# Kernel tuning notes

Measured on AMD Instinct MI355X. Metric: run time of the kernel, lower is better.

Reference implementation:

```python
import jax, jax.numpy as jnp
import numpy as np

TOP_K = 3
EPS = 1e-12  # F.normalize eps


def _lstm(x, W_ih, W_hh, b_ih, b_hh):
    # x: [B, S, I]; PyTorch gate order i, f, g, o; returns h sequence [B, S, H]
    B = x.shape[0]
    H = W_hh.shape[1]
    xs = jnp.swapaxes(x, 0, 1)  # [S, B, I]
    x_proj = xs @ W_ih.T + b_ih + b_hh  # [S, B, 4H]

    def step(carry, xp):
        h, c = carry
        gates = xp + h @ W_hh.T
        i, f, g, o = jnp.split(gates, 4, axis=-1)
        i = jax.nn.sigmoid(i); f = jax.nn.sigmoid(f)
        g = jnp.tanh(g); o = jax.nn.sigmoid(o)
        c = f * c + i * g
        h = o * jnp.tanh(c)
        return (h, c), h

    init = (jnp.zeros((B, H), x.dtype), jnp.zeros((B, H), x.dtype))
    _, hs = jax.lax.scan(step, init, x_proj)
    return jnp.swapaxes(hs, 0, 1)  # [B, S, H]


def setup_inputs() -> dict:
    key = jax.random.key(0)
    ks = jax.random.split(key, 16)
    B, S, I, H, M, N, O = 4, 256, 512, 1024, 256, 65536, 512
    sc = 0.02
    return {
        "x": jax.random.normal(ks[0], (B, S, I), jnp.float32),
        "keys": jax.random.normal(ks[1], (N, M), jnp.float32),
        "values": jax.random.normal(ks[2], (N, M), jnp.float32),
        "importance": jnp.ones((N,), jnp.float32),
        "W_ih": jax.random.normal(ks[3], (4 * H, I), jnp.float32) * sc,
        "W_hh": jax.random.normal(ks[4], (4 * H, H), jnp.float32) * sc,
        "b_ih": jnp.zeros((4 * H,), jnp.float32),
        "b_hh": jnp.zeros((4 * H,), jnp.float32),
        "Wq": jax.random.normal(ks[5], (M, H), jnp.float32) * sc,
        "bq": jnp.zeros((M,), jnp.float32),
        "Wa": jax.random.normal(ks[6], (1, M), jnp.float32) * sc,
        "ba": jnp.zeros((1,), jnp.float32),
        "Wc": jax.random.normal(ks[7], (M, M), jnp.float32) * sc,
        "bc": jnp.zeros((M,), jnp.float32),
        "Wo": jax.random.normal(ks[8], (O, H + M), jnp.float32) * sc,
        "bo": jnp.zeros((O,), jnp.float32),
    }


def reference(x, keys, values, importance, W_ih, W_hh, b_ih, b_hh,
              Wq, bq, Wa, ba, Wc, bc, Wo, bo):
    # Controller LSTM over the whole sequence
    h = _lstm(x, W_ih, W_hh, b_ih, b_hh)  # [B, S, H]

    # Query projection and cosine similarity against the memory keys
    q = h @ Wq.T + bq  # [B, S, M]
    qn = q / jnp.maximum(jnp.linalg.norm(q, axis=-1, keepdims=True), EPS)
    kn = keys / jnp.maximum(jnp.linalg.norm(keys, axis=-1, keepdims=True), EPS)
    sim = jnp.einsum("bsm,nm->bsn", qn, kn) * importance  # [B, S, N]

    # Top-k retrieval and value gather
    _, top_idx = jax.lax.top_k(sim, TOP_K)  # [B, S, k]
    retrieved = values[top_idx]  # [B, S, k, M]

    # Learned attention over retrieved memories
    att_logits = (retrieved @ Wa.T + ba)[..., 0]  # [B, S, k]
    att = jax.nn.softmax(att_logits, axis=-1)
    mem = jnp.einsum("bsk,bskm->bsm", att, retrieved)
    mem = mem @ Wc.T + bc  # combine_layer

    out = jnp.concatenate([h, mem], axis=-1) @ Wo.T + bo  # [B, S, O]
    return out
```

## Files before the change

### kernel.cpp

```cpp
#include <hip/hip_runtime.h>
#include <hip/hip_bf16.h>
#include <cstdint>
#include <cstddef>

#define BB 4
#define SS 256
#define ID 512
#define HD 1024
#define MD 256
#define NKEY 65536
#define OD 512
#define ROWS 1024
#define NWG_LSTM 256
#define NTH_LSTM 256
#define KPB 2048
#define KSPLITS (NKEY / KPB)

typedef __attribute__((ext_vector_type(8))) short bf16x8;
typedef __attribute__((ext_vector_type(4))) float f32x4;
typedef __attribute__((ext_vector_type(8))) unsigned short u16x8;

__global__ __launch_bounds__(256) void sgemm_nt(
    const float* __restrict__ A, int lda,
    const float* __restrict__ Bm, int ldb,
    float* __restrict__ C, int ldc, int K,
    const float* __restrict__ bias, const float* __restrict__ bias2,
    int accum)
{
    __shared__ float As[64][17];
    __shared__ float Bs[64][17];
    const int t = threadIdx.x;
    const int tx = t & 15, ty = t >> 4;
    const int bm = blockIdx.y << 6, bn = blockIdx.x << 6;
    const int lrow = t >> 2, lk4 = (t & 3) << 2;
    float acc[4][4] = {};

    for (int kb = 0; kb < K; kb += 16) {
        const float4 av = *(const float4*)&A[(size_t)(bm + lrow) * lda + kb + lk4];
        const float4 bv = *(const float4*)&Bm[(size_t)(bn + lrow) * ldb + kb + lk4];
        __syncthreads();
        As[lrow][lk4 + 0] = av.x; As[lrow][lk4 + 1] = av.y;
        As[lrow][lk4 + 2] = av.z; As[lrow][lk4 + 3] = av.w;
        Bs[lrow][lk4 + 0] = bv.x; Bs[lrow][lk4 + 1] = bv.y;
        Bs[lrow][lk4 + 2] = bv.z; Bs[lrow][lk4 + 3] = bv.w;
        __syncthreads();
#pragma unroll
        for (int k = 0; k < 16; ++k) {
            const float a0 = As[4 * ty + 0][k], a1 = As[4 * ty + 1][k];
            const float a2 = As[4 * ty + 2][k], a3 = As[4 * ty + 3][k];
            const float b0 = Bs[4 * tx + 0][k], b1 = Bs[4 * tx + 1][k];
            const float b2 = Bs[4 * tx + 2][k], b3 = Bs[4 * tx + 3][k];
            acc[0][0] += a0 * b0; acc[0][1] += a0 * b1; acc[0][2] += a0 * b2; acc[0][3] += a0 * b3;
            acc[1][0] += a1 * b0; acc[1][1] += a1 * b1; acc[1][2] += a1 * b2; acc[1][3] += a1 * b3;
            acc[2][0] += a2 * b0; acc[2][1] += a2 * b1; acc[2][2] += a2 * b2; acc[2][3] += a2 * b3;
            acc[3][0] += a3 * b0; acc[3][1] += a3 * b1; acc[3][2] += a3 * b2; acc[3][3] += a3 * b3;
        }
    }

#pragma unroll
    for (int i = 0; i < 4; ++i) {
        const int row = bm + 4 * ty + i;
        const int col = bn + 4 * tx;
        float4* cp = (float4*)&C[(size_t)row * ldc + col];
        float4 r;
        if (accum) {
            const float4 old = *cp;
            r.x = old.x + acc[i][0]; r.y = old.y + acc[i][1];
            r.z = old.z + acc[i][2]; r.w = old.w + acc[i][3];
        } else {
            float bx = bias[col + 0], by = bias[col + 1], bz = bias[col + 2], bw = bias[col + 3];
            if (bias2) { bx += bias2[col + 0]; by += bias2[col + 1]; bz += bias2[col + 2]; bw += bias2[col + 3]; }
            r.x = acc[i][0] + bx; r.y = acc[i][1] + by;
            r.z = acc[i][2] + bz; r.w = acc[i][3] + bw;
        }
        *cp = r;
    }
}

__global__ __launch_bounds__(256) void sgemm_nt_w(
    const float* __restrict__ A, const float* __restrict__ Bm,
    float* __restrict__ C, const float* __restrict__ bias, const float* __restrict__ bias2)
{
    __shared__ float As[16][64];
    __shared__ float Bs[16][128];
    const int t = threadIdx.x;
    const int tx = t & 15, ty = t >> 4;
    const int bm = blockIdx.y << 6, bn = blockIdx.x << 7;
    const int arow = t & 63, akq = t >> 6;
    const int brow = t & 127, bkq = t >> 7;
    float acc[4][8] = {};

    for (int kb = 0; kb < 512; kb += 16) {
        const float4 av  = *(const float4*)&A[(size_t)(bm + arow) * 512 + kb + (akq << 2)];
        const float4 bv0 = *(const float4*)&Bm[(size_t)(bn + brow) * 512 + kb + (bkq << 3)];
        const float4 bv1 = *(const float4*)&Bm[(size_t)(bn + brow) * 512 + kb + (bkq << 3) + 4];
        __syncthreads();
        As[(akq << 2) + 0][arow] = av.x; As[(akq << 2) + 1][arow] = av.y;
        As[(akq << 2) + 2][arow] = av.z; As[(akq << 2) + 3][arow] = av.w;
        Bs[(bkq << 3) + 0][brow] = bv0.x; Bs[(bkq << 3) + 1][brow] = bv0.y;
        Bs[(bkq << 3) + 2][brow] = bv0.z; Bs[(bkq << 3) + 3][brow] = bv0.w;
        Bs[(bkq << 3) + 4][brow] = bv1.x; Bs[(bkq << 3) + 5][brow] = bv1.y;
        Bs[(bkq << 3) + 6][brow] = bv1.z; Bs[(bkq << 3) + 7][brow] = bv1.w;
        __syncthreads();
#pragma unroll
        for (int k = 0; k < 16; ++k) {
            const float4 a  = *(const float4*)&As[k][ty << 2];
            const float4 b0 = *(const float4*)&Bs[k][tx << 3];
            const float4 b1 = *(const float4*)&Bs[k][(tx << 3) + 4];
            acc[0][0] += a.x * b0.x; acc[0][1] += a.x * b0.y; acc[0][2] += a.x * b0.z; acc[0][3] += a.x * b0.w;
            acc[0][4] += a.x * b1.x; acc[0][5] += a.x * b1.y; acc[0][6] += a.x * b1.z; acc[0][7] += a.x * b1.w;
            acc[1][0] += a.y * b0.x; acc[1][1] += a.y * b0.y; acc[1][2] += a.y * b0.z; acc[1][3] += a.y * b0.w;
            acc[1][4] += a.y * b1.x; acc[1][5] += a.y * b1.y; acc[1][6] += a.y * b1.z; acc[1][7] += a.y * b1.w;
            acc[2][0] += a.z * b0.x; acc[2][1] += a.z * b0.y; acc[2][2] += a.z * b0.z; acc[2][3] += a.z * b0.w;
            acc[2][4] += a.z * b1.x; acc[2][5] += a.z * b1.y; acc[2][6] += a.z * b1.z; acc[2][7] += a.z * b1.w;
            acc[3][0] += a.w * b0.x; acc[3][1] += a.w * b0.y; acc[3][2] += a.w * b0.z; acc[3][3] += a.w * b0.w;
            acc[3][4] += a.w * b1.x; acc[3][5] += a.w * b1.y; acc[3][6] += a.w * b1.z; acc[3][7] += a.w * b1.w;
        }
    }

#pragma unroll
    for (int i = 0; i < 4; ++i) {
        const int row = bm + (ty << 2) + i;
        const int col = bn + (tx << 3);
        float4 r0, r1;
        r0.x = acc[i][0] + bias[col + 0] + bias2[col + 0];
        r0.y = acc[i][1] + bias[col + 1] + bias2[col + 1];
        r0.z = acc[i][2] + bias[col + 2] + bias2[col + 2];
        r0.w = acc[i][3] + bias[col + 3] + bias2[col + 3];
        r1.x = acc[i][4] + bias[col + 4] + bias2[col + 4];
        r1.y = acc[i][5] + bias[col + 5] + bias2[col + 5];
        r1.z = acc[i][6] + bias[col + 6] + bias2[col + 6];
        r1.w = acc[i][7] + bias[col + 7] + bias2[col + 7];
        *(float4*)&C[(size_t)row * 4096 + col] = r0;
        *(float4*)&C[(size_t)row * 4096 + col + 4] = r1;
    }
}

__device__ inline unsigned pack_bf16(float a, float b) {
    return (__float_as_uint(a) >> 16) | (__float_as_uint(b) & 0xFFFF0000u);
}

__global__ void rownorm(const float* __restrict__ X, float* __restrict__ Xn, int nrows)
{
    const int row = blockIdx.x * 4 + (threadIdx.x >> 6);
    const int lane = threadIdx.x & 63;
    if (row >= nrows) return;
    float4 v = *(const float4*)&X[(size_t)row * 256 + (lane << 2)];
    float ss = v.x * v.x + v.y * v.y + v.z * v.z + v.w * v.w;
#pragma unroll
    for (int o = 1; o < 64; o <<= 1) ss += __shfl_xor(ss, o);
    const float sc = 1.f / fmaxf(sqrtf(ss), 1e-12f);
    v.x *= sc; v.y *= sc; v.z *= sc; v.w *= sc;
    *(float4*)&Xn[(size_t)row * 256 + (lane << 2)] = v;
}

__device__ inline float sigm_f(float x) { return 1.f / (1.f + __expf(-x)); }
__device__ inline float tanh_f(float x) { return 1.f - 2.f / (__expf(2.f * x) + 1.f); }

#define SUBSTEP(B, U, UN, C4, XPC) do {                                           \
    asm volatile("s_waitcnt vmcnt(3)" ::: "memory");                              \
    __builtin_amdgcn_sched_barrier(0);                                            \
    const unsigned* pb_ = rec + (slot << 12) + (B << 10) + (t << 2);              \
    while ((((U.x ^ st) | (U.y ^ st) | (U.z ^ st) | (U.w ^ st)) & 0xFFu) != 0u) { \
        __builtin_amdgcn_s_sleep(1);                                              \
        asm volatile("global_load_dwordx4 %0, %1, off sc0 sc1\n\ts_waitcnt vmcnt(0)" \
                     : "=&v"(U) : "v"(pb_) : "memory");                           \
    }                                                                             \
    {                                                                             \
        float4 hw_;                                                               \
        hw_.x = __uint_as_float(U.x & 0xFFFFFF00u);                               \
        hw_.y = __uint_as_float(U.y & 0xFFFFFF00u);                               \
        hw_.z = __uint_as_float(U.z & 0xFFFFFF00u);                               \
        hw_.w = __uint_as_float(U.w & 0xFFFFFF00u);                               \
        *(float4*)&h_lds[B][t << 2] = hw_;                                        \
    }                                                                             \
    asm volatile("s_waitcnt lgkmcnt(0)" ::: "memory");                            \
    __builtin_amdgcn_sched_barrier(0);                                            \
    __builtin_amdgcn_s_barrier();                                                 \
    {                                                                             \
        const unsigned* pn_ = rec + (((B == 3) ? (slot ^ 1) : slot) << 12)        \
                              + (((B + 1) & 3) << 10) + (t << 2);                 \
        asm volatile("global_load_dwordx4 %0, %1, off sc0 sc1"                    \
                     : "=&v"(UN) : "v"(pn_) : "memory");                          \
    }                                                                             \
    const float* hb_ = &h_lds[B][0];                                              \
    float ax_ = 0.f, ay_ = 0.f, az_ = 0.f, aw_ = 0.f;                             \
    _Pragma("unroll")                                                             \
    for (int j = 0; j < 16; ++j) {                                                \
        const float4 hv_ = *(const float4*)&hb_[(ksub << 2) + (j << 6)];          \
        ax_ += w4[j].x * hv_.x; ay_ += w4[j].y * hv_.y;                           \
        az_ += w4[j].z * hv_.z; aw_ += w4[j].w * hv_.w;                           \
    }                                                                             \
    float sm_ = (ax_ + ay_) + (az_ + aw_);                                        \
    sm_ += __shfl_xor(sm_, 1); sm_ += __shfl_xor(sm_, 2);                         \
    sm_ += __shfl_xor(sm_, 4); sm_ += __shfl_xor(sm_, 8);                         \
    sm_ += XPC;                                                                   \
    const float vi_ = __shfl(sm_, ksub);                                          \
    const float vf_ = __shfl(sm_, ksub + 16);                                     \
    const float vg_ = __shfl(sm_, ksub + 32);                                     \
    const float vo_ = __shfl(sm_, ksub + 48);                                     \
    const float iv_ = sigm_f(vi_), fv_ = sigm_f(vf_);                             \
    const float gv_ = tanh_f(vg_), ov_ = sigm_f(vo_);                             \
    C4 = fv_ * C4 + iv_ * gv_;                                                    \
    const float hvv_ = ov_ * tanh_f(C4);                                          \
    if (lane == 0) {                                                              \
        unsigned* dst_ = rec + ((slot ^ 1) << 12) + (B << 10) + unit;             \
        const unsigned uv_ = (__float_as_uint(hvv_) & 0xFFFFFF00u) |              \
                             ((unsigned)(s + 1) & 0xFFu);                         \
        float* ha_ = &h_all[(size_t)((B << 8) + s) * 1024 + unit];                \
        asm volatile("global_store_dword %0, %1, off sc0 sc1"                     \
                     :: "v"(dst_), "v"(uv_) : "memory");                          \
        asm volatile("global_store_dword %0, %1, off"                             \
                     :: "v"(ha_), "v"(hvv_) : "memory");                          \
    }                                                                             \
    {                                                                             \
        const float* px_ = &xp[(size_t)((B << 8) + sn) * 4096 + wrow];            \
        asm volatile("global_load_dword %0, %1, off"                              \
                     : "=&v"(XPC) : "v"(px_) : "memory");                         \
    }                                                                             \
} while (0)

__global__ __launch_bounds__(256) void lstm_kernel(
    const float* __restrict__ xp, const float* __restrict__ W_hh,
    unsigned* __restrict__ rec, float* __restrict__ h_all,
    const float* __restrict__ keys, const float* __restrict__ imp,
    float* __restrict__ rnk, unsigned short* __restrict__ kb)
{
    __shared__ float h_lds[4][1024];
    const int t = threadIdx.x;

    if (blockIdx.x >= NWG_LSTM) {
        const int base_row = (blockIdx.x - NWG_LSTM) << 8;
        const int lane = t & 63;
        for (int it = 0; it < 64; ++it) {
            const int row = base_row + (it << 2) + (t >> 6);
            float4 v = *(const float4*)&keys[(size_t)row * 256 + (lane << 2)];
            float ss = v.x * v.x + v.y * v.y + v.z * v.z + v.w * v.w;
#pragma unroll
            for (int o = 1; o < 64; o <<= 1) ss += __shfl_xor(ss, o);
            const float sc = imp[row] / fmaxf(sqrtf(ss), 1e-12f);
            if (lane == 0) rnk[row] = sc;
            if (kb) {
                uint2 p;
                p.x = pack_bf16(v.x * sc, v.y * sc);
                p.y = pack_bf16(v.z * sc, v.w * sc);
                *(uint2*)&kb[(size_t)row * 256 + (lane << 2)] = p;
            }
        }
        return;
    }

    const int wave = t >> 6, lane = t & 63;
    const int gt = lane >> 4, ksub = lane & 15;
    const int unit = (blockIdx.x << 2) + wave;
    const int wrow = (gt << 10) + unit;

    float4 w4[16];
#pragma unroll
    for (int j = 0; j < 16; ++j)
        w4[j] = *(const float4*)&W_hh[(size_t)wrow * 1024 + (ksub << 2) + (j << 6)];

    float c40 = 0.f, c41 = 0.f, c42 = 0.f, c43 = 0.f;
    float xpc0 = xp[(size_t)(0 * 256 + 0) * 4096 + wrow];
    float xpc1 = xp[(size_t)(1 * 256 + 0) * 4096 + wrow];
    float xpc2 = xp[(size_t)(2 * 256 + 0) * 4096 + wrow];
    float xpc3 = xp[(size_t)(3 * 256 + 0) * 4096 + wrow];

    uint4 u0 = make_uint4(~0u, ~0u, ~0u, ~0u);
    uint4 u1 = u0, u2 = u0, u3 = u0;

    {
        const unsigned* p00 = rec + (t << 2);
        asm volatile("global_load_dwordx4 %0, %1, off sc0 sc1\n\ts_waitcnt vmcnt(0)"
                     : "=&v"(u0) : "v"(p00) : "memory");
        __builtin_amdgcn_sched_barrier(0);
    }

    for (int s = 0; s < 256; ++s) {
        const int slot = s & 1;
        const unsigned st = (unsigned)s & 0xFFu;
        const int sn = (s < 255) ? s + 1 : 255;
        SUBSTEP(0, u0, u1, c40, xpc0);
        SUBSTEP(1, u1, u2, c41, xpc1);
        SUBSTEP(2, u2, u3, c42, xpc2);
        SUBSTEP(3, u3, u0, c43, xpc3);
    }
}

#define SWAP1(A, B, IA, IB) { float _t = A; A = B; B = _t; int _u = IA; IA = IB; IB = _u; }
#define INS8G(P, V, ID) do {                                          \
    const float _v = (V); const int _id = (ID);                       \
    if (_v > P##v7) {                                                 \
        P##v7 = _v; P##i7 = _id;                                      \
        if (P##v7 > P##v6) SWAP1(P##v6, P##v7, P##i6, P##i7);         \
        if (P##v6 > P##v5) SWAP1(P##v5, P##v6, P##i5, P##i6);         \
        if (P##v5 > P##v4) SWAP1(P##v4, P##v5, P##i4, P##i5);         \
        if (P##v4 > P##v3) SWAP1(P##v3, P##v4, P##i3, P##i4);         \
        if (P##v3 > P##v2) SWAP1(P##v2, P##v3, P##i2, P##i3);         \
        if (P##v2 > P##v1) SWAP1(P##v1, P##v2, P##i1, P##i2);         \
        if (P##v1 > P##v0) SWAP1(P##v0, P##v1, P##i0, P##i1);         \
    }                                                                 \
} while (0)
#define DECL8(P) float P##v0=-3e38f,P##v1=-3e38f,P##v2=-3e38f,P##v3=-3e38f, \
                       P##v4=-3e38f,P##v5=-3e38f,P##v6=-3e38f,P##v7=-3e38f; \
                 int P##i0=0x7fffffff,P##i1=0x7fffffff,P##i2=0x7fffffff,P##i3=0x7fffffff, \
                     P##i4=0x7fffffff,P##i5=0x7fffffff,P##i6=0x7fffffff,P##i7=0x7fffffff;

__global__ __launch_bounds__(256) void sim_mfma_b(
    const float* __restrict__ qn, const unsigned short* __restrict__ kb,
    float* __restrict__ part_v8, int* __restrict__ part_i8)
{
    __shared__ unsigned short k_lds[64 * 264];
    __shared__ float cand_v[256 * 8];
    __shared__ int   cand_i[256 * 8];
    const int t = threadIdx.x;
    const int wave = t >> 6, lane = t & 63;
    const int ks = blockIdx.x, qs = blockIdx.y;
    const int key_base = ks * KPB;
    const int q0 = qs << 6;
    const int qrow = q0 + (wave << 4) + (lane & 15);
    const int kg = lane >> 4;

    bf16x8 bq[8];
#pragma unroll
    for (int kc = 0; kc < 8; ++kc) {
        const float* qp = &qn[(size_t)qrow * 256 + (kc << 5) + (kg << 3)];
        const float4 f0 = *(const float4*)qp;
        const float4 f1 = *(const float4*)(qp + 4);
        union { unsigned int u[4]; bf16x8 h; } cv;
        cv.u[0] = pack_bf16(f0.x, f0.y);
        cv.u[1] = pack_bf16(f0.z, f0.w);
        cv.u[2] = pack_bf16(f1.x, f1.y);
        cv.u[3] = pack_bf16(f1.z, f1.w);
        bq[kc] = cv.h;
    }

    DECL8(t)

    const int srow = t >> 2, scol0 = (t & 3) << 6;

    for (int stg = 0; stg < KPB / 64; ++stg) {
        __syncthreads();
        {
            const unsigned short* kp = &kb[(size_t)(key_base + (stg << 6) + srow) * 256 + scol0];
#pragma unroll
            for (int i = 0; i < 8; ++i)
                *(u16x8*)&k_lds[srow * 264 + scol0 + (i << 3)] = *(const u16x8*)(kp + (i << 3));
        }
        __syncthreads();

#pragma unroll
        for (int kt = 0; kt < 4; ++kt) {
            f32x4 a0 = {0.f, 0.f, 0.f, 0.f};
            f32x4 a1 = {0.f, 0.f, 0.f, 0.f};
#pragma unroll
            for (int kc = 0; kc < 4; ++kc) {
                const bf16x8 af = *(const bf16x8*)&k_lds[((kt << 4) + (lane & 15)) * 264 +
                                                         (kc << 5) + (kg << 3)];
                a0 = __builtin_amdgcn_mfma_f32_16x16x32_bf16(af, bq[kc], a0, 0, 0, 0);
            }
#pragma unroll
            for (int kc = 4; kc < 8; ++kc) {
                const bf16x8 af = *(const bf16x8*)&k_lds[((kt << 4) + (lane & 15)) * 264 +
                                                         (kc << 5) + (kg << 3)];
                a1 = __builtin_amdgcn_mfma_f32_16x16x32_bf16(af, bq[kc], a1, 0, 0, 0);
            }
            const int kidx = key_base + (stg << 6) + (kt << 4) + (kg << 2);
            INS8G(t, a0[0] + a1[0], kidx + 0);
            INS8G(t, a0[1] + a1[1], kidx + 1);
            INS8G(t, a0[2] + a1[2], kidx + 2);
            INS8G(t, a0[3] + a1[3], kidx + 3);
        }
    }

    __syncthreads();
    cand_v[t * 8 + 0] = tv0; cand_i[t * 8 + 0] = ti0;
    cand_v[t * 8 + 1] = tv1; cand_i[t * 8 + 1] = ti1;
    cand_v[t * 8 + 2] = tv2; cand_i[t * 8 + 2] = ti2;
    cand_v[t * 8 + 3] = tv3; cand_i[t * 8 + 3] = ti3;
    cand_v[t * 8 + 4] = tv4; cand_i[t * 8 + 4] = ti4;
    cand_v[t * 8 + 5] = tv5; cand_i[t * 8 + 5] = ti5;
    cand_v[t * 8 + 6] = tv6; cand_i[t * 8 + 6] = ti6;
    cand_v[t * 8 + 7] = tv7; cand_i[t * 8 + 7] = ti7;
    __syncthreads();
    if (t < 64) {
        DECL8(m)
        const int w = t >> 4, c = t & 15;
        for (int g = 0; g < 4; ++g) {
            const int src = ((w << 6) + c + (g << 4)) * 8;
            for (int r = 0; r < 8; ++r)
                INS8G(m, cand_v[src + r], cand_i[src + r]);
        }
        const size_t base = (size_t)(q0 + t) * (KSPLITS * 8) + ks * 8;
        part_v8[base + 0] = mv0; part_i8[base + 0] = mi0;
        part_v8[base + 1] = mv1; part_i8[base + 1] = mi1;
        part_v8[base + 2] = mv2; part_i8[base + 2] = mi2;
        part_v8[base + 3] = mv3; part_i8[base + 3] = mi3;
        part_v8[base + 4] = mv4; part_i8[base + 4] = mi4;
        part_v8[base + 5] = mv5; part_i8[base + 5] = mi5;
        part_v8[base + 6] = mv6; part_i8[base + 6] = mi6;
        part_v8[base + 7] = mv7; part_i8[base + 7] = mi7;
    }
}

__global__ __launch_bounds__(256) void sim_mfma_f(
    const float* __restrict__ qn, const float* __restrict__ keys,
    const float* __restrict__ rnk, float* __restrict__ part_v8, int* __restrict__ part_i8)
{
    __shared__ unsigned short k_lds[64 * 264];
    __shared__ float cand_v[256 * 8];
    __shared__ int   cand_i[256 * 8];
    const int t = threadIdx.x;
    const int wave = t >> 6, lane = t & 63;
    const int ks = blockIdx.x, qs = blockIdx.y;
    const int key_base = ks * KPB;
    const int q0 = qs << 6;
    const int qrow = q0 + (wave << 4) + (lane & 15);
    const int kg = lane >> 4;

    bf16x8 bq[8];
#pragma unroll
    for (int kc = 0; kc < 8; ++kc) {
        const float* qp = &qn[(size_t)qrow * 256 + (kc << 5) + (kg << 3)];
        const float4 f0 = *(const float4*)qp;
        const float4 f1 = *(const float4*)(qp + 4);
        union { unsigned int u[4]; bf16x8 h; } cv;
        cv.u[0] = pack_bf16(f0.x, f0.y);
        cv.u[1] = pack_bf16(f0.z, f0.w);
        cv.u[2] = pack_bf16(f1.x, f1.y);
        cv.u[3] = pack_bf16(f1.z, f1.w);
        bq[kc] = cv.h;
    }

    DECL8(t)

    for (int stg = 0; stg < KPB / 64; ++stg) {
        __syncthreads();
#pragma unroll
        for (int i = 0; i < 8; ++i) {
            const int g = (i << 11) + (t << 3);
            const int row = g >> 8, col = g & 255;
            const int krow = key_base + (stg << 6) + row;
            const float sc = rnk[krow];
            const float* kp = &keys[(size_t)krow * 256 + col];
            float4 f0 = *(const float4*)kp;
            float4 f1 = *(const float4*)(kp + 4);
            f0.x *= sc; f0.y *= sc; f0.z *= sc; f0.w *= sc;
            f1.x *= sc; f1.y *= sc; f1.z *= sc; f1.w *= sc;
            union { unsigned int u[4]; u16x8 h; } cv;
            cv.u[0] = pack_bf16(f0.x, f0.y);
            cv.u[1] = pack_bf16(f0.z, f0.w);
            cv.u[2] = pack_bf16(f1.x, f1.y);
            cv.u[3] = pack_bf16(f1.z, f1.w);
            *(u16x8*)&k_lds[row * 264 + col] = cv.h;
        }
        __syncthreads();

#pragma unroll
        for (int kt = 0; kt < 4; ++kt) {
            f32x4 a0 = {0.f, 0.f, 0.f, 0.f};
            f32x4 a1 = {0.f, 0.f, 0.f, 0.f};
#pragma unroll
            for (int kc = 0; kc < 4; ++kc) {
                const bf16x8 af = *(const bf16x8*)&k_lds[((kt << 4) + (lane & 15)) * 264 +
                                                         (kc << 5) + (kg << 3)];
                a0 = __builtin_amdgcn_mfma_f32_16x16x32_bf16(af, bq[kc], a0, 0, 0, 0);
            }
#pragma unroll
            for (int kc = 4; kc < 8; ++kc) {
                const bf16x8 af = *(const bf16x8*)&k_lds[((kt << 4) + (lane & 15)) * 264 +
                                                         (kc << 5) + (kg << 3)];
                a1 = __builtin_amdgcn_mfma_f32_16x16x32_bf16(af, bq[kc], a1, 0, 0, 0);
            }
            const int kidx = key_base + (stg << 6) + (kt << 4) + (kg << 2);
            INS8G(t, a0[0] + a1[0], kidx + 0);
            INS8G(t, a0[1] + a1[1], kidx + 1);
            INS8G(t, a0[2] + a1[2], kidx + 2);
            INS8G(t, a0[3] + a1[3], kidx + 3);
        }
    }

    __syncthreads();
    cand_v[t * 8 + 0] = tv0; cand_i[t * 8 + 0] = ti0;
    cand_v[t * 8 + 1] = tv1; cand_i[t * 8 + 1] = ti1;
    cand_v[t * 8 + 2] = tv2; cand_i[t * 8 + 2] = ti2;
    cand_v[t * 8 + 3] = tv3; cand_i[t * 8 + 3] = ti3;
    cand_v[t * 8 + 4] = tv4; cand_i[t * 8 + 4] = ti4;
    cand_v[t * 8 + 5] = tv5; cand_i[t * 8 + 5] = ti5;
    cand_v[t * 8 + 6] = tv6; cand_i[t * 8 + 6] = ti6;
    cand_v[t * 8 + 7] = tv7; cand_i[t * 8 + 7] = ti7;
    __syncthreads();
    if (t < 64) {
        DECL8(m)
        const int w = t >> 4, c = t & 15;
        for (int g = 0; g < 4; ++g) {
            const int src = ((w << 6) + c + (g << 4)) * 8;
            for (int r = 0; r < 8; ++r)
                INS8G(m, cand_v[src + r], cand_i[src + r]);
        }
        const size_t base = (size_t)(q0 + t) * (KSPLITS * 8) + ks * 8;
        part_v8[base + 0] = mv0; part_i8[base + 0] = mi0;
        part_v8[base + 1] = mv1; part_i8[base + 1] = mi1;
        part_v8[base + 2] = mv2; part_i8[base + 2] = mi2;
        part_v8[base + 3] = mv3; part_i8[base + 3] = mi3;
        part_v8[base + 4] = mv4; part_i8[base + 4] = mi4;
        part_v8[base + 5] = mv5; part_i8[base + 5] = mi5;
        part_v8[base + 6] = mv6; part_i8[base + 6] = mi6;
        part_v8[base + 7] = mv7; part_i8[base + 7] = mi7;
    }
}

__global__ void cand_merge(const float* __restrict__ part_v8, const int* __restrict__ part_i8,
                           int* __restrict__ cand8_i)
{
    const int q = blockIdx.x * 256 + threadIdx.x;
    if (q >= ROWS) return;
    DECL8(c)
    for (int j = 0; j < KSPLITS * 8; ++j)
        INS8G(c, part_v8[(size_t)q * (KSPLITS * 8) + j], part_i8[(size_t)q * (KSPLITS * 8) + j]);
    cand8_i[q * 8 + 0] = ci0; cand8_i[q * 8 + 1] = ci1;
    cand8_i[q * 8 + 2] = ci2; cand8_i[q * 8 + 3] = ci3;
    cand8_i[q * 8 + 4] = ci4; cand8_i[q * 8 + 5] = ci5;
    cand8_i[q * 8 + 6] = ci6; cand8_i[q * 8 + 7] = ci7;
}

__global__ void rescore_gather(const float* __restrict__ qn, const float* __restrict__ keys,
                               const float* __restrict__ rnk, const int* __restrict__ cand8_i,
                               const float* __restrict__ values, const float* __restrict__ Wa,
                               const float* __restrict__ ba, float* __restrict__ mem_raw)
{
    const int q = blockIdx.x;
    const int lane = threadIdx.x;
    const float4 qv = *(const float4*)&qn[(size_t)q * 256 + (lane << 2)];
    float s0, s1, s2, s3, s4, s5, s6, s7;
    int j0, j1, j2, j3, j4, j5, j6, j7;
#define RES(R, S, J) { J = cand8_i[q * 8 + R]; \
    const float4 kv = *(const float4*)&keys[(size_t)J * 256 + (lane << 2)]; \
    float d = qv.x * kv.x + qv.y * kv.y + qv.z * kv.z + qv.w * kv.w; \
    d += __shfl_xor(d, 1); d += __shfl_xor(d, 2); d += __shfl_xor(d, 4); \
    d += __shfl_xor(d, 8); d += __shfl_xor(d, 16); d += __shfl_xor(d, 32); \
    S = d * rnk[J]; }
    RES(0, s0, j0) RES(1, s1, j1) RES(2, s2, j2) RES(3, s3, j3)
    RES(4, s4, j4) RES(5, s5, j5) RES(6, s6, j6) RES(7, s7, j7)
#undef RES
    int top[3];
#define BET(SV, JV) if (SV > bv || (SV == bv && JV < bi)) { bv = SV; bi = JV; }
#pragma unroll
    for (int k = 0; k < 3; ++k) {
        float bv = s0; int bi = j0;
        BET(s1, j1) BET(s2, j2) BET(s3, j3) BET(s4, j4)
        BET(s5, j5) BET(s6, j6) BET(s7, j7)
        top[k] = bi;
        if (j0 == bi) s0 = -3e38f;
        if (j1 == bi) s1 = -3e38f;
        if (j2 == bi) s2 = -3e38f;
        if (j3 == bi) s3 = -3e38f;
        if (j4 == bi) s4 = -3e38f;
        if (j5 == bi) s5 = -3e38f;
        if (j6 == bi) s6 = -3e38f;
        if (j7 == bi) s7 = -3e38f;
    }
#undef BET
    const float4 wa = *(const float4*)&Wa[lane << 2];
    float4 vr[3];
    float lg[3];
#pragma unroll
    for (int r = 0; r < 3; ++r) {
        const float4 v = *(const float4*)&values[(size_t)top[r] * 256 + (lane << 2)];
        vr[r] = v;
        float d = v.x * wa.x + v.y * wa.y + v.z * wa.z + v.w * wa.w;
#pragma unroll
        for (int o = 1; o < 64; o <<= 1) d += __shfl_xor(d, o);
        lg[r] = d + ba[0];
    }
    const float mx = fmaxf(lg[0], fmaxf(lg[1], lg[2]));
    float e0 = __expf(lg[0] - mx), e1 = __expf(lg[1] - mx), e2 = __expf(lg[2] - mx);
    const float inv = 1.f / (e0 + e1 + e2);
    e0 *= inv; e1 *= inv; e2 *= inv;
    float4 m;
    m.x = e0 * vr[0].x + e1 * vr[1].x + e2 * vr[2].x;
    m.y = e0 * vr[0].y + e1 * vr[1].y + e2 * vr[2].y;
    m.z = e0 * vr[0].z + e1 * vr[1].z + e2 * vr[2].z;
    m.w = e0 * vr[0].w + e1 * vr[1].w + e2 * vr[2].w;
    *(float4*)&mem_raw[(size_t)q * 256 + (lane << 2)] = m;
}

extern "C" void kernel_launch(void* const* d_in, const int* in_sizes, int n_in,
                              void* d_out, int out_size, void* d_ws, size_t ws_size,
                              hipStream_t stream)
{
    (void)in_sizes; (void)n_in; (void)out_size;
    const float* x     = (const float*)d_in[0];
    const float* keys  = (const float*)d_in[1];
    const float* values= (const float*)d_in[2];
    const float* imp   = (const float*)d_in[3];
    const float* W_ih  = (const float*)d_in[4];
    const float* W_hh  = (const float*)d_in[5];
    const float* b_ih  = (const float*)d_in[6];
    const float* b_hh  = (const float*)d_in[7];
    const float* Wq    = (const float*)d_in[8];
    const float* bq    = (const float*)d_in[9];
    const float* Wa    = (const float*)d_in[10];
    const float* ba    = (const float*)d_in[11];
    const float* Wc    = (const float*)d_in[12];
    const float* bc    = (const float*)d_in[13];
    const float* Wo    = (const float*)d_in[14];
    const float* bo    = (const float*)d_in[15];
    float* out = (float*)d_out;

    float* ws = (float*)d_ws;
    size_t o = 0;
    float* xp      = ws + o; o += (size_t)1024 * 4096;
    float* h_all   = ws + o; o += (size_t)1024 * 1024;
    unsigned* rec  = (unsigned*)(ws + o); o += 2 * 4096;
    float* rnk     = ws + o; o += NKEY;
    float* qbuf    = ws + o; o += (size_t)ROWS * 256;
    float* qn      = ws + o; o += (size_t)ROWS * 256;
    float* part_v8 = ws + o; o += (size_t)ROWS * KSPLITS * 8;
    int*   part_i8 = (int*)(ws + o); o += (size_t)ROWS * KSPLITS * 8;
    int*   cand8_i = (int*)(ws + o); o += ROWS * 8;
    float* mem_raw = ws + o; o += (size_t)ROWS * 256;
    float* memb    = ws + o; o += (size_t)ROWS * 256;
    unsigned short* kb = (unsigned short*)(ws + o);
    const size_t need_bf16 = (o + (size_t)NKEY * 256 / 2) * sizeof(float);
    const bool use_bf16 = ws_size >= need_bf16;

    hipMemsetAsync(rec, 0, 2 * 4096 * 4, stream);

    sgemm_nt_w<<<dim3(32, 16), 256, 0, stream>>>(x, W_ih, xp, b_ih, b_hh);

    lstm_kernel<<<2 * NWG_LSTM, NTH_LSTM, 0, stream>>>(
        xp, W_hh, rec, h_all, keys, imp, rnk, use_bf16 ? kb : nullptr);

    sgemm_nt<<<dim3(4, 16), 256, 0, stream>>>(h_all, HD, Wq, HD, qbuf, MD, HD, bq, nullptr, 0);

    rownorm<<<ROWS / 4, 256, 0, stream>>>(qbuf, qn, ROWS);

    if (use_bf16)
        sim_mfma_b<<<dim3(KSPLITS, 16), 256, 0, stream>>>(qn, kb, part_v8, part_i8);
    else
        sim_mfma_f<<<dim3(KSPLITS, 16), 256, 0, stream>>>(qn, keys, rnk, part_v8, part_i8);
    cand_merge<<<ROWS / 256, 256, 0, stream>>>(part_v8, part_i8, cand8_i);
    rescore_gather<<<ROWS, 64, 0, stream>>>(qn, keys, rnk, cand8_i, values, Wa, ba, mem_raw);

    sgemm_nt<<<dim3(4, 16), 256, 0, stream>>>(mem_raw, MD, Wc, MD, memb, MD, MD, bc, nullptr, 0);

    sgemm_nt<<<dim3(8, 16), 256, 0, stream>>>(h_all, HD, Wo, HD + MD, out, OD, HD, bo, nullptr, 0);
    sgemm_nt<<<dim3(8, 16), 256, 0, stream>>>(memb, MD, Wo + HD, HD + MD, out, OD, MD, nullptr, nullptr, 1);
}
```

Before: 1.325 ms.

## Widen bf16 similarity blocks to 128 queries and parallelize candidate merge

The bf16 similarity kernel now runs 512 threads (8 waves) per block covering 128 query rows, so each key tile staged in LDS is reused by twice as many queries and global key traffic is halved. Candidate LDS buffers are aliased onto the key tile to keep shared memory small. The candidate merge kernel changes from one thread per query scanning 256 partials serially to 8 threads per query, each merging 32 partials, followed by an LDS-based final merge. The trade-off is half as many blocks in the sim grid, which may lower occupancy and parallelism, plus a larger per-block final reduction.

```diff
diff --git a/kernel.cpp b/kernel.cpp
--- a/kernel.cpp
+++ b/kernel.cpp
@@ -306,9 +306,106 @@
                  int P##i0=0x7fffffff,P##i1=0x7fffffff,P##i2=0x7fffffff,P##i3=0x7fffffff, \
                      P##i4=0x7fffffff,P##i5=0x7fffffff,P##i6=0x7fffffff,P##i7=0x7fffffff;
 
-__global__ __launch_bounds__(256) void sim_mfma_b(
+__global__ __launch_bounds__(512) void sim_mfma_b8(
     const float* __restrict__ qn, const unsigned short* __restrict__ kb,
     float* __restrict__ part_v8, int* __restrict__ part_i8)
+{
+    __shared__ unsigned short k_lds[64 * 264];
+    const int t = threadIdx.x;
+    const int wave = t >> 6, lane = t & 63;
+    const int ks = blockIdx.x, qs = blockIdx.y;
+    const int key_base = ks * KPB;
+    const int q0 = qs << 7;
+    const int qrow = q0 + (wave << 4) + (lane & 15);
+    const int kg = lane >> 4;
+
+    bf16x8 bq[8];
+#pragma unroll
+    for (int kc = 0; kc < 8; ++kc) {
+        const float* qp = &qn[(size_t)qrow * 256 + (kc << 5) + (kg << 3)];
+        const float4 f0 = *(const float4*)qp;
+        const float4 f1 = *(const float4*)(qp + 4);
+        union { unsigned int u[4]; bf16x8 h; } cv;
+        cv.u[0] = pack_bf16(f0.x, f0.y);
+        cv.u[1] = pack_bf16(f0.z, f0.w);
+        cv.u[2] = pack_bf16(f1.x, f1.y);
+        cv.u[3] = pack_bf16(f1.z, f1.w);
+        bq[kc] = cv.h;
+    }
+
+    DECL8(t)
+
+    const int srow = t >> 3, scol0 = (t & 7) << 5;
+
+    for (int stg = 0; stg < KPB / 64; ++stg) {
+        __syncthreads();
+        {
+            const unsigned short* kp = &kb[(size_t)(key_base + (stg << 6) + srow) * 256 + scol0];
+#pragma unroll
+            for (int i = 0; i < 4; ++i)
+                *(u16x8*)&k_lds[srow * 264 + scol0 + (i << 3)] = *(const u16x8*)(kp + (i << 3));
+        }
+        __syncthreads();
+
+#pragma unroll
+        for (int kt = 0; kt < 4; ++kt) {
+            f32x4 a0 = {0.f, 0.f, 0.f, 0.f};
+            f32x4 a1 = {0.f, 0.f, 0.f, 0.f};
+#pragma unroll
+            for (int kc = 0; kc < 4; ++kc) {
+                const bf16x8 af = *(const bf16x8*)&k_lds[((kt << 4) + (lane & 15)) * 264 +
+                                                         (kc << 5) + (kg << 3)];
+                a0 = __builtin_amdgcn_mfma_f32_16x16x32_bf16(af, bq[kc], a0, 0, 0, 0);
+            }
+#pragma unroll
+            for (int kc = 4; kc < 8; ++kc) {
+                const bf16x8 af = *(const bf16x8*)&k_lds[((kt << 4) + (lane & 15)) * 264 +
+                                                         (kc << 5) + (kg << 3)];
+                a1 = __builtin_amdgcn_mfma_f32_16x16x32_bf16(af, bq[kc], a1, 0, 0, 0);
+            }
+            const int kidx = key_base + (stg << 6) + (kt << 4) + (kg << 2);
+            INS8G(t, a0[0] + a1[0], kidx + 0);
+            INS8G(t, a0[1] + a1[1], kidx + 1);
+            INS8G(t, a0[2] + a1[2], kidx + 2);
+            INS8G(t, a0[3] + a1[3], kidx + 3);
+        }
+    }
+
+    float* cand_v = (float*)k_lds;
+    int*   cand_i = (int*)(k_lds + 8192);
+    __syncthreads();
+    cand_v[t * 8 + 0] = tv0; cand_i[t * 8 + 0] = ti0;
+    cand_v[t * 8 + 1] = tv1; cand_i[t * 8 + 1] = ti1;
+    cand_v[t * 8 + 2] = tv2; cand_i[t * 8 + 2] = ti2;
+    cand_v[t * 8 + 3] = tv3; cand_i[t * 8 + 3] = ti3;
+    cand_v[t * 8 + 4] = tv4; cand_i[t * 8 + 4] = ti4;
+    cand_v[t * 8 + 5] = tv5; cand_i[t * 8 + 5] = ti5;
+    cand_v[t * 8 + 6] = tv6; cand_i[t * 8 + 6] = ti6;
+    cand_v[t * 8 + 7] = tv7; cand_i[t * 8 + 7] = ti7;
+    __syncthreads();
+    if (t < 128) {
+        DECL8(m)
+        const int w = t >> 4, c = t & 15;
+        for (int g = 0; g < 4; ++g) {
+            const int src = ((w << 6) + (g << 4) + c) * 8;
+            for (int r = 0; r < 8; ++r)
+                INS8G(m, cand_v[src + r], cand_i[src + r]);
+        }
+        const size_t base = (size_t)(q0 + t) * (KSPLITS * 8) + ks * 8;
+        part_v8[base + 0] = mv0; part_i8[base + 0] = mi0;
+        part_v8[base + 1] = mv1; part_i8[base + 1] = mi1;
+        part_v8[base + 2] = mv2; part_i8[base + 2] = mi2;
+        part_v8[base + 3] = mv3; part_i8[base + 3] = mi3;
+        part_v8[base + 4] = mv4; part_i8[base + 4] = mi4;
+        part_v8[base + 5] = mv5; part_i8[base + 5] = mi5;
+        part_v8[base + 6] = mv6; part_i8[base + 6] = mi6;
+        part_v8[base + 7] = mv7; part_i8[base + 7] = mi7;
+    }
+}
+
+__global__ __launch_bounds__(256) void sim_mfma_f(
+    const float* __restrict__ qn, const float* __restrict__ keys,
+    const float* __restrict__ rnk, float* __restrict__ part_v8, int* __restrict__ part_i8)
 {
     __shared__ unsigned short k_lds[64 * 264];
     __shared__ float cand_v[256 * 8];
@@ -337,15 +434,25 @@
 
     DECL8(t)
 
-    const int srow = t >> 2, scol0 = (t & 3) << 6;
-
     for (int stg = 0; stg < KPB / 64; ++stg) {
         __syncthreads();
-        {
-            const unsigned short* kp = &kb[(size_t)(key_base + (stg << 6) + srow) * 256 + scol0];
-#pragma unroll
-            for (int i = 0; i < 8; ++i)
-                *(u16x8*)&k_lds[srow * 264 + scol0 + (i << 3)] = *(const u16x8*)(kp + (i << 3));
+#pragma unroll
+        for (int i = 0; i < 8; ++i) {
+            const int g = (i << 11) + (t << 3);
+            const int row = g >> 8, col = g & 255;
+            const int krow = key_base + (stg << 6) + row;
+            const float sc = rnk[krow];
+            const float* kp = &keys[(size_t)krow * 256 + col];
+            float4 f0 = *(const float4*)kp;
+            float4 f1 = *(const float4*)(kp + 4);
+            f0.x *= sc; f0.y *= sc; f0.z *= sc; f0.w *= sc;
+            f1.x *= sc; f1.y *= sc; f1.z *= sc; f1.w *= sc;
+            union { unsigned int u[4]; u16x8 h; } cv;
+            cv.u[0] = pack_bf16(f0.x, f0.y);
+            cv.u[1] = pack_bf16(f0.z, f0.w);
+            cv.u[2] = pack_bf16(f1.x, f1.y);
+            cv.u[3] = pack_bf16(f1.z, f1.w);
+            *(u16x8*)&k_lds[row * 264 + col] = cv.h;
         }
         __syncthreads();
 
@@ -403,125 +510,40 @@
     }
 }
 
-__global__ __launch_bounds__(256) void sim_mfma_f(
-    const float* __restrict__ qn, const float* __restrict__ keys,
-    const float* __restrict__ rnk, float* __restrict__ part_v8, int* __restrict__ part_i8)
-{
-    __shared__ unsigned short k_lds[64 * 264];
-    __shared__ float cand_v[256 * 8];
-    __shared__ int   cand_i[256 * 8];
+__global__ __launch_bounds__(256) void cand_merge(
+    const float* __restrict__ part_v8, const int* __restrict__ part_i8,
+    int* __restrict__ cand8_i)
+{
+    __shared__ float pv[256 * 8];
+    __shared__ int   pi[256 * 8];
     const int t = threadIdx.x;
-    const int wave = t >> 6, lane = t & 63;
-    const int ks = blockIdx.x, qs = blockIdx.y;
-    const int key_base = ks * KPB;
-    const int q0 = qs << 6;
-    const int qrow = q0 + (wave << 4) + (lane & 15);
-    const int kg = lane >> 4;
-
-    bf16x8 bq[8];
-#pragma unroll
-    for (int kc = 0; kc < 8; ++kc) {
-        const float* qp = &qn[(size_t)qrow * 256 + (kc << 5) + (kg << 3)];
-        const float4 f0 = *(const float4*)qp;
-        const float4 f1 = *(const float4*)(qp + 4);
-        union { unsigned int u[4]; bf16x8 h; } cv;
-        cv.u[0] = pack_bf16(f0.x, f0.y);
-        cv.u[1] = pack_bf16(f0.z, f0.w);
-        cv.u[2] = pack_bf16(f1.x, f1.y);
-        cv.u[3] = pack_bf16(f1.z, f1.w);
-        bq[kc] = cv.h;
-    }
-
-    DECL8(t)
-
-    for (int stg = 0; stg < KPB / 64; ++stg) {
-        __syncthreads();
-#pragma unroll
-        for (int i = 0; i < 8; ++i) {
-            const int g = (i << 11) + (t << 3);
-            const int row = g >> 8, col = g & 255;
-            const int krow = key_base + (stg << 6) + row;
-            const float sc = rnk[krow];
-            const float* kp = &keys[(size_t)krow * 256 + col];
-            float4 f0 = *(const float4*)kp;
-            float4 f1 = *(const float4*)(kp + 4);
-            f0.x *= sc; f0.y *= sc; f0.z *= sc; f0.w *= sc;
-            f1.x *= sc; f1.y *= sc; f1.z *= sc; f1.w *= sc;
-            union { unsigned int u[4]; u16x8 h; } cv;
-            cv.u[0] = pack_bf16(f0.x, f0.y);
-            cv.u[1] = pack_bf16(f0.z, f0.w);
-            cv.u[2] = pack_bf16(f1.x, f1.y);
-            cv.u[3] = pack_bf16(f1.z, f1.w);
-            *(u16x8*)&k_lds[row * 264 + col] = cv.h;
-        }
-        __syncthreads();
-
-#pragma unroll
-        for (int kt = 0; kt < 4; ++kt) {
-            f32x4 a0 = {0.f, 0.f, 0.f, 0.f};
-            f32x4 a1 = {0.f, 0.f, 0.f, 0.f};
-#pragma unroll
-            for (int kc = 0; kc < 4; ++kc) {
-                const bf16x8 af = *(const bf16x8*)&k_lds[((kt << 4) + (lane & 15)) * 264 +
-                                                         (kc << 5) + (kg << 3)];
-                a0 = __builtin_amdgcn_mfma_f32_16x16x32_bf16(af, bq[kc], a0, 0, 0, 0);
-            }
-#pragma unroll
-            for (int kc = 4; kc < 8; ++kc) {
-                const bf16x8 af = *(const bf16x8*)&k_lds[((kt << 4) + (lane & 15)) * 264 +
-                                                         (kc << 5) + (kg << 3)];
-                a1 = __builtin_amdgcn_mfma_f32_16x16x32_bf16(af, bq[kc], a1, 0, 0, 0);
-            }
-            const int kidx = key_base + (stg << 6) + (kt << 4) + (kg << 2);
-            INS8G(t, a0[0] + a1[0], kidx + 0);
-            INS8G(t, a0[1] + a1[1], kidx + 1);
-            INS8G(t, a0[2] + a1[2], kidx + 2);
-            INS8G(t, a0[3] + a1[3], kidx + 3);
-        }
-    }
-
+    const int qq = t >> 3, sl = t & 7;
+    const int q = (blockIdx.x << 5) + qq;
+    {
+        DECL8(p)
+        const size_t base = (size_t)q * (KSPLITS * 8) + sl * 32;
+        for (int j = 0; j < 32; ++j)
+            INS8G(p, part_v8[base + j], part_i8[base + j]);
+        pv[t * 8 + 0] = pv0; pi[t * 8 + 0] = pi0;
+        pv[t * 8 + 1] = pv1; pi[t * 8 + 1] = pi1;
+        pv[t * 8 + 2] = pv2; pi[t * 8 + 2] = pi2;
+        pv[t * 8 + 3] = pv3; pi[t * 8 + 3] = pi3;
+        pv[t * 8 + 4] = pv4; pi[t * 8 + 4] = pi4;
+        pv[t * 8 + 5] = pv5; pi[t * 8 + 5] = pi5;
+        pv[t * 8 + 6] = pv6; pi[t * 8 + 6] = pi6;
+        pv[t * 8 + 7] = pv7; pi[t * 8 + 7] = pi7;
+    }
     __syncthreads();
-    cand_v[t * 8 + 0] = tv0; cand_i[t * 8 + 0] = ti0;
-    cand_v[t * 8 + 1] = tv1; cand_i[t * 8 + 1] = ti1;
-    cand_v[t * 8 + 2] = tv2; cand_i[t * 8 + 2] = ti2;
-    cand_v[t * 8 + 3] = tv3; cand_i[t * 8 + 3] = ti3;
-    cand_v[t * 8 + 4] = tv4; cand_i[t * 8 + 4] = ti4;
-    cand_v[t * 8 + 5] = tv5; cand_i[t * 8 + 5] = ti5;
-    cand_v[t * 8 + 6] = tv6; cand_i[t * 8 + 6] = ti6;
-    cand_v[t * 8 + 7] = tv7; cand_i[t * 8 + 7] = ti7;
-    __syncthreads();
-    if (t < 64) {
-        DECL8(m)
-        const int w = t >> 4, c = t & 15;
-        for (int g = 0; g < 4; ++g) {
-            const int src = ((w << 6) + c + (g << 4)) * 8;
-            for (int r = 0; r < 8; ++r)
-                INS8G(m, cand_v[src + r], cand_i[src + r]);
-        }
-        const size_t base = (size_t)(q0 + t) * (KSPLITS * 8) + ks * 8;
-        part_v8[base + 0] = mv0; part_i8[base + 0] = mi0;
-        part_v8[base + 1] = mv1; part_i8[base + 1] = mi1;
-        part_v8[base + 2] = mv2; part_i8[base + 2] = mi2;
-        part_v8[base + 3] = mv3; part_i8[base + 3] = mi3;
-        part_v8[base + 4] = mv4; part_i8[base + 4] = mi4;
-        part_v8[base + 5] = mv5; part_i8[base + 5] = mi5;
-        part_v8[base + 6] = mv6; part_i8[base + 6] = mi6;
-        part_v8[base + 7] = mv7; part_i8[base + 7] = mi7;
-    }
-}
-
-__global__ void cand_merge(const float* __restrict__ part_v8, const int* __restrict__ part_i8,
-                           int* __restrict__ cand8_i)
-{
-    const int q = blockIdx.x * 256 + threadIdx.x;
-    if (q >= ROWS) return;
-    DECL8(c)
-    for (int j = 0; j < KSPLITS * 8; ++j)
-        INS8G(c, part_v8[(size_t)q * (KSPLITS * 8) + j], part_i8[(size_t)q * (KSPLITS * 8) + j]);
-    cand8_i[q * 8 + 0] = ci0; cand8_i[q * 8 + 1] = ci1;
-    cand8_i[q * 8 + 2] = ci2; cand8_i[q * 8 + 3] = ci3;
-    cand8_i[q * 8 + 4] = ci4; cand8_i[q * 8 + 5] = ci5;
-    cand8_i[q * 8 + 6] = ci6; cand8_i[q * 8 + 7] = ci7;
+    if (sl == 0) {
+        DECL8(c)
+        const int b0 = (qq << 3) * 8;
+        for (int j = 0; j < 64; ++j)
+            INS8G(c, pv[b0 + j], pi[b0 + j]);
+        cand8_i[q * 8 + 0] = ci0; cand8_i[q * 8 + 1] = ci1;
+        cand8_i[q * 8 + 2] = ci2; cand8_i[q * 8 + 3] = ci3;
+        cand8_i[q * 8 + 4] = ci4; cand8_i[q * 8 + 5] = ci5;
+        cand8_i[q * 8 + 6] = ci6; cand8_i[q * 8 + 7] = ci7;
+    }
 }
 
 __global__ void rescore_gather(const float* __restrict__ qn, const float* __restrict__ keys,
@@ -637,10 +659,10 @@
     rownorm<<<ROWS / 4, 256, 0, stream>>>(qbuf, qn, ROWS);
 
     if (use_bf16)
-        sim_mfma_b<<<dim3(KSPLITS, 16), 256, 0, stream>>>(qn, kb, part_v8, part_i8);
+        sim_mfma_b8<<<dim3(KSPLITS, 8), 512, 0, stream>>>(qn, kb, part_v8, part_i8);
     else
         sim_mfma_f<<<dim3(KSPLITS, 16), 256, 0, stream>>>(qn, keys, rnk, part_v8, part_i8);
-    cand_merge<<<ROWS / 256, 256, 0, stream>>>(part_v8, part_i8, cand8_i);
+    cand_merge<<<32, 256, 0, stream>>>(part_v8, part_i8, cand8_i);
     rescore_gather<<<ROWS, 64, 0, stream>>>(qn, keys, rnk, cand8_i, values, Wa, ba, mem_raw);
 
     sgemm_nt<<<dim3(4, 16), 256, 0, stream>>>(mem_raw, MD, Wc, MD, memb, MD, MD, bc, nullptr, 0);
```

Measured after the change: 1.262 ms. 4.8% less time.
